# Kernel tuning notes

Measured on AMD Instinct MI355X. Metric: run time of the kernel, lower is better.

## Reference

```python
import jax, jax.numpy as jnp
import numpy as np

B, L, C = 32, 4096, 512
H = 8            # num_heads
WS = 16          # window size
HID = 4 * C      # mlp hidden
D = C // H       # head dim
SCALE = D ** -0.5
EPS = 1e-3       # keras LayerNormalization default epsilon


def _ln(x, g, b):
    m = jnp.mean(x, axis=-1, keepdims=True)
    v = jnp.var(x, axis=-1, keepdims=True)
    return (x - m) * jax.lax.rsqrt(v + EPS) * g + b


def setup_inputs() -> dict:
    key = jax.random.key(0)
    ks = jax.random.split(key, 12)
    s = 0.02
    return {
        "x": jax.random.normal(ks[0], (B, L, C), dtype=jnp.float32),
        "g1": jnp.ones((C,), jnp.float32),
        "b1": jnp.zeros((C,), jnp.float32),
        "w_qkv": jax.random.normal(ks[1], (C, 3 * C), jnp.float32) * s,
        "b_qkv": jnp.zeros((3 * C,), jnp.float32),
        "bias_table": jax.random.normal(ks[2], (2 * WS - 1, H), jnp.float32) * s,
        "w_proj": jax.random.normal(ks[3], (C, C), jnp.float32) * s,
        "b_proj": jnp.zeros((C,), jnp.float32),
        "g2": jnp.ones((C,), jnp.float32),
        "b2": jnp.zeros((C,), jnp.float32),
        "w_fc1": jax.random.normal(ks[4], (C, HID), jnp.float32) * s,
        "b_fc1": jnp.zeros((HID,), jnp.float32),
        "w_fc2": jax.random.normal(ks[5], (HID, C), jnp.float32) * s,
        "b_fc2": jnp.zeros((C,), jnp.float32),
    }


def reference(x, g1, b1, w_qkv, b_qkv, bias_table, w_proj, b_proj,
              g2, b2, w_fc1, b_fc1, w_fc2, b_fc2):
    shortcut = x
    h = _ln(x, g1, b1)
    # window partition: (B, L, C) -> (B*L/WS, WS, C); shift_size=0 so no roll
    xw = h.reshape(-1, WS, C)
    # qkv projection
    qkv = (xw @ w_qkv + b_qkv).reshape(-1, WS, 3, H, D)
    qkv = jnp.transpose(qkv, (2, 0, 3, 1, 4))  # (3, nB, H, WS, D)
    q, k, v = qkv[0] * SCALE, qkv[1], qkv[2]
    attn = jnp.einsum('bhqd,bhkd->bhqk', q, k)
    # relative position bias
    rel_idx = jnp.arange(WS)[:, None] - jnp.arange(WS)[None, :] + WS - 1  # (WS, WS)
    bias = jnp.transpose(bias_table[rel_idx], (2, 0, 1))  # (H, WS, WS)
    attn = jax.nn.softmax(attn + bias[None], axis=-1)
    out = jnp.einsum('bhqk,bhkd->bqhd', attn, v).reshape(-1, WS, C)
    out = out @ w_proj + b_proj
    # window reverse
    out = out.reshape(B, L, C)
    x = shortcut + out
    # MLP block (exact gelu matches tf.nn.gelu default approximate=False)
    h2 = _ln(x, g2, b2)
    h2 = jax.nn.gelu(h2 @ w_fc1 + b_fc1, approximate=False)
    h2 = h2 @ w_fc2 + b_fc2
    return x + h2
```

## Files before the change

kernel.cpp:

```cpp
#include <hip/hip_runtime.h>
#include <hip/hip_bf16.h>

typedef short bf16x8 __attribute__((ext_vector_type(8)));
typedef float f32x4 __attribute__((ext_vector_type(4)));

#define GLDS16(gp, lp)                                                         \
  __builtin_amdgcn_global_load_lds(                                            \
      (const __attribute__((address_space(1))) void*)(gp),                     \
      (__attribute__((address_space(3))) void*)(lp), 16, 0, 0)

static __device__ __forceinline__ unsigned short f2bf(float f) {
  unsigned u = __float_as_uint(f);
  u += 0x7fffu + ((u >> 16) & 1u);
  return (unsigned short)(u >> 16);
}

__global__ __launch_bounds__(256) void wt_transpose_kernel(
    const float* __restrict__ w, unsigned short* __restrict__ wt, int K, int N) {
  __shared__ float tile[32][33];
  const int n0 = blockIdx.x * 32, k0 = blockIdx.y * 32;
  const int tx = threadIdx.x & 31, ty = threadIdx.x >> 5;
#pragma unroll
  for (int i = 0; i < 4; ++i) {
    const int k = ty + i * 8;
    tile[k][tx] = w[(size_t)(k0 + k) * N + n0 + tx];
  }
  __syncthreads();
#pragma unroll
  for (int i = 0; i < 4; ++i) {
    const int n = ty + i * 8;
    wt[(size_t)(n0 + n) * K + k0 + tx] = f2bf(tile[tx][n]);
  }
}

__global__ __launch_bounds__(256) void ln_bf16_kernel(
    const float* __restrict__ x, const float* __restrict__ gw,
    const float* __restrict__ bw, unsigned short* __restrict__ out) {
  const int wv = threadIdx.x >> 6, lane = threadIdx.x & 63;
  const size_t t = (size_t)blockIdx.x * 4 + wv;
  const float4* xr = (const float4*)(x + t * 512);
  const float4 v0 = xr[lane * 2];
  const float4 v1 = xr[lane * 2 + 1];
  float s = v0.x + v0.y + v0.z + v0.w + v1.x + v1.y + v1.z + v1.w;
  float ss = v0.x * v0.x + v0.y * v0.y + v0.z * v0.z + v0.w * v0.w +
             v1.x * v1.x + v1.y * v1.y + v1.z * v1.z + v1.w * v1.w;
#pragma unroll
  for (int m = 1; m < 64; m <<= 1) {
    s += __shfl_xor(s, m);
    ss += __shfl_xor(ss, m);
  }
  const float mean = s * (1.0f / 512.0f);
  const float var = fmaxf(ss * (1.0f / 512.0f) - mean * mean, 0.0f);
  const float rstd = rsqrtf(var + 1e-3f);
  const float4* gp = (const float4*)gw;
  const float4* bp = (const float4*)bw;
  const float4 g0 = gp[lane * 2], g1 = gp[lane * 2 + 1];
  const float4 b0 = bp[lane * 2], b1 = bp[lane * 2 + 1];
  uint4 o;
  o.x = (unsigned)f2bf((v0.x - mean) * rstd * g0.x + b0.x) |
        ((unsigned)f2bf((v0.y - mean) * rstd * g0.y + b0.y) << 16);
  o.y = (unsigned)f2bf((v0.z - mean) * rstd * g0.z + b0.z) |
        ((unsigned)f2bf((v0.w - mean) * rstd * g0.w + b0.w) << 16);
  o.z = (unsigned)f2bf((v1.x - mean) * rstd * g1.x + b1.x) |
        ((unsigned)f2bf((v1.y - mean) * rstd * g1.y + b1.y) << 16);
  o.w = (unsigned)f2bf((v1.z - mean) * rstd * g1.z + b1.z) |
        ((unsigned)f2bf((v1.w - mean) * rstd * g1.w + b1.w) << 16);
  *(uint4*)(out + t * 512 + lane * 8) = o;
}

template <int EPI>
__global__ __launch_bounds__(256) void gemm_bf16_kernel(
    const unsigned short* __restrict__ A, const unsigned short* __restrict__ Bt,
    const float* __restrict__ bias, const float* __restrict__ resid,
    void* __restrict__ outv, int M, int N, int K) {
  __shared__ __align__(16) unsigned short sA[128 * 64];
  __shared__ __align__(16) unsigned short sB[128 * 64];
  const int nTn = N >> 7;
  const int nwg = gridDim.x;
  const int bid = blockIdx.x;
  const int swz = (bid & 7) * (nwg >> 3) + (bid >> 3);
  const int tm = swz / nTn, tn = swz % nTn;
  const int lane = threadIdx.x & 63, wv = threadIdx.x >> 6;
  const int wm = wv >> 1, wn = wv & 1;
  const int lr = lane & 15, lg = lane >> 4;
  const unsigned short* Ab =
      A + (size_t)tm * 128 * K + (size_t)(lane >> 3) * K + (lane & 7) * 8;
  const unsigned short* Bb =
      Bt + (size_t)tn * 128 * K + (size_t)(lane >> 3) * K + (lane & 7) * 8;
  f32x4 acc[4][4] = {};
  for (int kt = 0; kt < K; kt += 64) {
#pragma unroll
    for (int i = 0; i < 4; ++i) {
      const int r0 = (wv * 4 + i) * 8;
      GLDS16(Ab + (size_t)r0 * K + kt, &sA[r0 * 64]);
      GLDS16(Bb + (size_t)r0 * K + kt, &sB[r0 * 64]);
    }
    __syncthreads();
#pragma unroll
    for (int kk = 0; kk < 2; ++kk) {
      bf16x8 af[4], bf[4];
#pragma unroll
      for (int m = 0; m < 4; ++m)
        af[m] = *(const bf16x8*)&sA[(wm * 64 + m * 16 + lr) * 64 + kk * 32 + lg * 8];
#pragma unroll
      for (int n = 0; n < 4; ++n)
        bf[n] = *(const bf16x8*)&sB[(wn * 64 + n * 16 + lr) * 64 + kk * 32 + lg * 8];
#pragma unroll
      for (int m = 0; m < 4; ++m)
#pragma unroll
        for (int n = 0; n < 4; ++n)
          acc[m][n] = __builtin_amdgcn_mfma_f32_16x16x32_bf16(af[m], bf[n],
                                                              acc[m][n], 0, 0, 0);
    }
    __syncthreads();
  }
  const int row0 = tm * 128 + wm * 64 + lg * 4;
  const int col0 = tn * 128 + wn * 64 + lr;
#pragma unroll
  for (int n = 0; n < 4; ++n) {
    const int col = col0 + n * 16;
    const float bs = bias[col];
#pragma unroll
    for (int m = 0; m < 4; ++m) {
#pragma unroll
      for (int r = 0; r < 4; ++r) {
        const size_t idx = (size_t)(row0 + m * 16 + r) * N + col;
        float v = acc[m][n][r] + bs;
        if (EPI == 1) {
          ((float*)outv)[idx] = v + resid[idx];
        } else if (EPI == 2) {
          v = 0.5f * v * (1.0f + erff(v * 0.70710678118f));
          ((unsigned short*)outv)[idx] = f2bf(v);
        } else {
          ((unsigned short*)outv)[idx] = f2bf(v);
        }
      }
    }
  }
}

__global__ __launch_bounds__(256) void attn_kernel(
    const unsigned short* __restrict__ qkv,
    const float* __restrict__ bias_table, unsigned short* __restrict__ out) {
  __shared__ __align__(16) unsigned short sVt[4][64 * 16];
  __shared__ __align__(16) unsigned short sP[4][16 * 16];
  const int wv = threadIdx.x >> 6, lane = threadIdx.x & 63;
  const int task = blockIdx.x * 4 + wv;
  const int w = task >> 3, h = task & 7;
  const int c = lane & 15, g = lane >> 4;
  const unsigned short* base =
      qkv + (size_t)w * 16 * 1536 + (size_t)c * 1536 + h * 64;
  const bf16x8 qf0 = *(const bf16x8*)(base + g * 8);
  const bf16x8 qf1 = *(const bf16x8*)(base + 32 + g * 8);
  const bf16x8 kf0 = *(const bf16x8*)(base + 512 + g * 8);
  const bf16x8 kf1 = *(const bf16x8*)(base + 512 + 32 + g * 8);
  const bf16x8 vf0 = *(const bf16x8*)(base + 1024 + g * 8);
  const bf16x8 vf1 = *(const bf16x8*)(base + 1024 + 32 + g * 8);
  unsigned short* vt = sVt[wv];
#pragma unroll
  for (int j = 0; j < 8; ++j) vt[(g * 8 + j) * 16 + c] = (unsigned short)vf0[j];
#pragma unroll
  for (int j = 0; j < 8; ++j) vt[(32 + g * 8 + j) * 16 + c] = (unsigned short)vf1[j];
  f32x4 s = {0.f, 0.f, 0.f, 0.f};
  s = __builtin_amdgcn_mfma_f32_16x16x32_bf16(qf0, kf0, s, 0, 0, 0);
  s = __builtin_amdgcn_mfma_f32_16x16x32_bf16(qf1, kf1, s, 0, 0, 0);
  float p[4];
#pragma unroll
  for (int r = 0; r < 4; ++r) {
    const int q = g * 4 + r;
    p[r] = s[r] * 0.125f + bias_table[(q - c + 15) * 8 + h];
  }
#pragma unroll
  for (int r = 0; r < 4; ++r) {
    float m = p[r];
    m = fmaxf(m, __shfl_xor(m, 1));
    m = fmaxf(m, __shfl_xor(m, 2));
    m = fmaxf(m, __shfl_xor(m, 4));
    m = fmaxf(m, __shfl_xor(m, 8));
    const float e = __expf(p[r] - m);
    float t = e;
    t += __shfl_xor(t, 1);
    t += __shfl_xor(t, 2);
    t += __shfl_xor(t, 4);
    t += __shfl_xor(t, 8);
    p[r] = e * __builtin_amdgcn_rcpf(t);
  }
  unsigned short* pb = sP[wv];
#pragma unroll
  for (int r = 0; r < 4; ++r) pb[(g * 4 + r) * 16 + c] = f2bf(p[r]);
  __syncthreads();
  bf16x8 pf;
#pragma unroll
  for (int j = 0; j < 8; ++j) pf[j] = 0;
  if (g < 2) pf = *(const bf16x8*)&pb[c * 16 + g * 8];
  const int kk0 = (g & 1) * 8;
  unsigned short* ob = out + (size_t)w * 16 * 512 + (size_t)c * 512 + h * 64;
#pragma unroll
  for (int ch = 0; ch < 4; ++ch) {
    const bf16x8 av = *(const bf16x8*)&vt[(ch * 16 + c) * 16 + kk0];
    f32x4 o = {0.f, 0.f, 0.f, 0.f};
    o = __builtin_amdgcn_mfma_f32_16x16x32_bf16(av, pf, o, 0, 0, 0);
    ushort4 pk;
    pk.x = f2bf(o[0]);
    pk.y = f2bf(o[1]);
    pk.z = f2bf(o[2]);
    pk.w = f2bf(o[3]);
    *(ushort4*)(ob + ch * 16 + g * 4) = pk;
  }
}

extern "C" void kernel_launch(void* const* d_in, const int* in_sizes, int n_in,
                              void* d_out, int out_size, void* d_ws,
                              size_t ws_size, hipStream_t stream) {
  (void)in_sizes; (void)n_in; (void)out_size;
  const float* x      = (const float*)d_in[0];
  const float* g1     = (const float*)d_in[1];
  const float* b1     = (const float*)d_in[2];
  const float* w_qkv  = (const float*)d_in[3];
  const float* b_qkv  = (const float*)d_in[4];
  const float* btab   = (const float*)d_in[5];
  const float* w_proj = (const float*)d_in[6];
  const float* b_proj = (const float*)d_in[7];
  const float* g2     = (const float*)d_in[8];
  const float* b2     = (const float*)d_in[9];
  const float* w_fc1  = (const float*)d_in[10];
  const float* b_fc1  = (const float*)d_in[11];
  const float* w_fc2  = (const float*)d_in[12];
  const float* b_fc2  = (const float*)d_in[13];
  float* out = (float*)d_out;

  char* ws = (char*)d_ws;
  const size_t OFF_BIG = 134217728ull;
  const size_t OFF_ATT = OFF_BIG + 402653184ull;
  const size_t OFF_WT  = OFF_BIG + 536870912ull;
  if (ws_size < OFF_WT + 6291456ull) return;
  unsigned short* hbuf   = (unsigned short*)(ws);
  unsigned short* qkvhid = (unsigned short*)(ws + OFF_BIG);
  unsigned short* attnb  = (unsigned short*)(ws + OFF_ATT);
  unsigned short* wqkvT  = (unsigned short*)(ws + OFF_WT);
  unsigned short* wprojT = wqkvT + 512 * 1536;
  unsigned short* wfc1T  = wprojT + 512 * 512;
  unsigned short* wfc2T  = wfc1T + 512 * 2048;

  wt_transpose_kernel<<<dim3(1536 / 32, 512 / 32), 256, 0, stream>>>(w_qkv, wqkvT, 512, 1536);
  wt_transpose_kernel<<<dim3(512 / 32, 512 / 32), 256, 0, stream>>>(w_proj, wprojT, 512, 512);
  wt_transpose_kernel<<<dim3(2048 / 32, 512 / 32), 256, 0, stream>>>(w_fc1, wfc1T, 512, 2048);
  wt_transpose_kernel<<<dim3(512 / 32, 2048 / 32), 256, 0, stream>>>(w_fc2, wfc2T, 2048, 512);

  ln_bf16_kernel<<<32768, 256, 0, stream>>>(x, g1, b1, hbuf);
  gemm_bf16_kernel<0><<<12288, 256, 0, stream>>>(hbuf, wqkvT, b_qkv, nullptr,
                                                 qkvhid, 131072, 1536, 512);
  attn_kernel<<<16384, 256, 0, stream>>>(qkvhid, btab, attnb);
  gemm_bf16_kernel<1><<<4096, 256, 0, stream>>>(attnb, wprojT, b_proj, x, out,
                                                131072, 512, 512);
  ln_bf16_kernel<<<32768, 256, 0, stream>>>(out, g2, b2, hbuf);
  gemm_bf16_kernel<2><<<16384, 256, 0, stream>>>(hbuf, wfc1T, b_fc1, nullptr,
                                                 qkvhid, 131072, 2048, 512);
  gemm_bf16_kernel<1><<<4096, 256, 0, stream>>>(qkvhid, wfc2T, b_fc2, out, out,
                                                131072, 512, 2048);
}
```

Measured before the change: 2.363 ms.

## Replace 128x128 GEMM with 256x256 double-buffered, swizzled 8-wave pipelined kernel

```diff
diff --git a/kernel.cpp b/kernel.cpp
--- a/kernel.cpp
+++ b/kernel.cpp
@@ -8,6 +8,10 @@
   __builtin_amdgcn_global_load_lds(                                            \
       (const __attribute__((address_space(1))) void*)(gp),                     \
       (__attribute__((address_space(3))) void*)(lp), 16, 0, 0)
+#define BAR() __builtin_amdgcn_s_barrier()
+#define SCHED0() __builtin_amdgcn_sched_barrier(0)
+#define PRIO(p) __builtin_amdgcn_s_setprio(p)
+#define MFMA(a, b, c) __builtin_amdgcn_mfma_f32_16x16x32_bf16((a), (b), (c), 0, 0, 0)
 
 static __device__ __forceinline__ unsigned short f2bf(float f) {
   unsigned u = __float_as_uint(f);
@@ -69,59 +73,145 @@
 }
 
 template <int EPI>
-__global__ __launch_bounds__(256) void gemm_bf16_kernel(
+__global__ __launch_bounds__(512, 2) void gemm256_kernel(
     const unsigned short* __restrict__ A, const unsigned short* __restrict__ Bt,
     const float* __restrict__ bias, const float* __restrict__ resid,
     void* __restrict__ outv, int M, int N, int K) {
-  __shared__ __align__(16) unsigned short sA[128 * 64];
-  __shared__ __align__(16) unsigned short sB[128 * 64];
-  const int nTn = N >> 7;
-  const int nwg = gridDim.x;
-  const int bid = blockIdx.x;
+  __shared__ __align__(16) unsigned short lds[2][2][256 * 64];
+  const int NT = K >> 6;
+  const int nTn = N >> 8;
+  const int bid = blockIdx.x, nwg = gridDim.x;
   const int swz = (bid & 7) * (nwg >> 3) + (bid >> 3);
-  const int tm = swz / nTn, tn = swz % nTn;
-  const int lane = threadIdx.x & 63, wv = threadIdx.x >> 6;
-  const int wm = wv >> 1, wn = wv & 1;
-  const int lr = lane & 15, lg = lane >> 4;
-  const unsigned short* Ab =
-      A + (size_t)tm * 128 * K + (size_t)(lane >> 3) * K + (lane & 7) * 8;
-  const unsigned short* Bb =
-      Bt + (size_t)tn * 128 * K + (size_t)(lane >> 3) * K + (lane & 7) * 8;
-  f32x4 acc[4][4] = {};
-  for (int kt = 0; kt < K; kt += 64) {
-#pragma unroll
-    for (int i = 0; i < 4; ++i) {
-      const int r0 = (wv * 4 + i) * 8;
-      GLDS16(Ab + (size_t)r0 * K + kt, &sA[r0 * 64]);
-      GLDS16(Bb + (size_t)r0 * K + kt, &sB[r0 * 64]);
-    }
-    __syncthreads();
-#pragma unroll
-    for (int kk = 0; kk < 2; ++kk) {
-      bf16x8 af[4], bf[4];
-#pragma unroll
-      for (int m = 0; m < 4; ++m)
-        af[m] = *(const bf16x8*)&sA[(wm * 64 + m * 16 + lr) * 64 + kk * 32 + lg * 8];
-#pragma unroll
-      for (int n = 0; n < 4; ++n)
-        bf[n] = *(const bf16x8*)&sB[(wn * 64 + n * 16 + lr) * 64 + kk * 32 + lg * 8];
-#pragma unroll
-      for (int m = 0; m < 4; ++m)
-#pragma unroll
-        for (int n = 0; n < 4; ++n)
-          acc[m][n] = __builtin_amdgcn_mfma_f32_16x16x32_bf16(af[m], bf[n],
-                                                              acc[m][n], 0, 0, 0);
-    }
-    __syncthreads();
-  }
-  const int row0 = tm * 128 + wm * 64 + lg * 4;
-  const int col0 = tn * 128 + wn * 64 + lr;
+  const int tmr = (swz / nTn) * 256, tnr = (swz % nTn) * 256;
+  const int tid = threadIdx.x;
+  const int l = tid & 63, w = tid >> 6;
+  const int lr = l & 15, lg = l >> 4, x = lr & 7;
+  const int wm = w >> 2, wn = w & 3;
+  const int l8 = l >> 3;
+  const int coff = ((l & 7) ^ l8) * 8;
+  const int k0 = (lg ^ x) * 8, k1 = k0 ^ 32;
+  const int abase = (wm * 128 + lr) * 64;
+  const int bbase = (wn * 64 + lr) * 64;
+
+  f32x4 acc[8][4] = {};
+
+#define STAGE_A(buf, row0, kt)                                                  \
+  do {                                                                          \
+    const int kte_ = (kt) < NT ? (kt) : (kt) - NT;                              \
+    const unsigned short* s_ =                                                  \
+        A + (size_t)(tmr + (row0) + w * 16 + l8) * K + kte_ * 64 + coff;        \
+    GLDS16(s_, &lds[buf][0][((row0) + w * 16) * 64]);                           \
+    GLDS16(s_ + (size_t)8 * K, &lds[buf][0][((row0) + w * 16 + 8) * 64]);       \
+  } while (0)
+#define STAGE_B(buf, row0, kt)                                                  \
+  do {                                                                          \
+    const int kte_ = (kt) < NT ? (kt) : (kt) - NT;                              \
+    const unsigned short* s_ =                                                  \
+        Bt + (size_t)(tnr + (row0) + w * 16 + l8) * K + kte_ * 64 + coff;       \
+    GLDS16(s_, &lds[buf][1][((row0) + w * 16) * 64]);                           \
+    GLDS16(s_ + (size_t)8 * K, &lds[buf][1][((row0) + w * 16 + 8) * 64]);       \
+  } while (0)
+
+  STAGE_A(0, 0, 0);
+  STAGE_B(0, 0, 0);
+  STAGE_A(0, 128, 0);
+  STAGE_B(0, 128, 0);
+  STAGE_A(1, 0, 1);
+  STAGE_B(1, 0, 1);
+  asm volatile("s_waitcnt vmcnt(4)" ::: "memory");
+  BAR();
+  SCHED0();
+
+  for (int g = 0; g < NT; ++g) {
+    const int cb = g & 1, nb = cb ^ 1;
+    const unsigned short* sA = &lds[cb][0][0];
+    const unsigned short* sB = &lds[cb][1][0];
+    bf16x8 a0[4][2], a1[4][2], b0[2][2], b1[2][2];
+#pragma unroll
+    for (int m = 0; m < 4; ++m) {
+      a0[m][0] = *(const bf16x8*)(sA + abase + m * 1024 + k0);
+      a0[m][1] = *(const bf16x8*)(sA + abase + m * 1024 + k1);
+    }
+#pragma unroll
+    for (int n = 0; n < 2; ++n) {
+      b0[n][0] = *(const bf16x8*)(sB + bbase + n * 1024 + k0);
+      b0[n][1] = *(const bf16x8*)(sB + bbase + n * 1024 + k1);
+    }
+    STAGE_A(nb, 128, g + 1);
+    BAR();
+    PRIO(1);
+#pragma unroll
+    for (int m = 0; m < 4; ++m)
+#pragma unroll
+      for (int n = 0; n < 2; ++n) {
+        acc[m][n] = MFMA(a0[m][0], b0[n][0], acc[m][n]);
+        acc[m][n] = MFMA(a0[m][1], b0[n][1], acc[m][n]);
+      }
+    PRIO(0);
+    BAR();
+    SCHED0();
+#pragma unroll
+    for (int n = 0; n < 2; ++n) {
+      b1[n][0] = *(const bf16x8*)(sB + bbase + 2048 + n * 1024 + k0);
+      b1[n][1] = *(const bf16x8*)(sB + bbase + 2048 + n * 1024 + k1);
+    }
+    STAGE_B(nb, 128, g + 1);
+    BAR();
+    PRIO(1);
+#pragma unroll
+    for (int m = 0; m < 4; ++m)
+#pragma unroll
+      for (int n = 0; n < 2; ++n) {
+        acc[m][2 + n] = MFMA(a0[m][0], b1[n][0], acc[m][2 + n]);
+        acc[m][2 + n] = MFMA(a0[m][1], b1[n][1], acc[m][2 + n]);
+      }
+    PRIO(0);
+    BAR();
+    SCHED0();
+#pragma unroll
+    for (int m = 0; m < 4; ++m) {
+      a1[m][0] = *(const bf16x8*)(sA + abase + 4096 + m * 1024 + k0);
+      a1[m][1] = *(const bf16x8*)(sA + abase + 4096 + m * 1024 + k1);
+    }
+    BAR();
+    PRIO(1);
+#pragma unroll
+    for (int m = 0; m < 4; ++m)
+#pragma unroll
+      for (int n = 0; n < 2; ++n) {
+        acc[4 + m][2 + n] = MFMA(a1[m][0], b1[n][0], acc[4 + m][2 + n]);
+        acc[4 + m][2 + n] = MFMA(a1[m][1], b1[n][1], acc[4 + m][2 + n]);
+      }
+    PRIO(0);
+    BAR();
+    SCHED0();
+    STAGE_A(cb, 0, g + 2);
+    STAGE_B(cb, 0, g + 2);
+    asm volatile("s_waitcnt vmcnt(4)" ::: "memory");
+    BAR();
+    PRIO(1);
+#pragma unroll
+    for (int m = 0; m < 4; ++m)
+#pragma unroll
+      for (int n = 0; n < 2; ++n) {
+        acc[4 + m][n] = MFMA(a1[m][0], b0[n][0], acc[4 + m][n]);
+        acc[4 + m][n] = MFMA(a1[m][1], b0[n][1], acc[4 + m][n]);
+      }
+    PRIO(0);
+    BAR();
+    SCHED0();
+  }
+#undef STAGE_A
+#undef STAGE_B
+
+  const int row0 = tmr + wm * 128 + lg * 4;
+  const int col0 = tnr + wn * 64 + lr;
 #pragma unroll
   for (int n = 0; n < 4; ++n) {
     const int col = col0 + n * 16;
     const float bs = bias[col];
 #pragma unroll
-    for (int m = 0; m < 4; ++m) {
+    for (int m = 0; m < 8; ++m) {
 #pragma unroll
       for (int r = 0; r < 4; ++r) {
         const size_t idx = (size_t)(row0 + m * 16 + r) * N + col;
@@ -162,8 +252,8 @@
 #pragma unroll
   for (int j = 0; j < 8; ++j) vt[(32 + g * 8 + j) * 16 + c] = (unsigned short)vf1[j];
   f32x4 s = {0.f, 0.f, 0.f, 0.f};
-  s = __builtin_amdgcn_mfma_f32_16x16x32_bf16(qf0, kf0, s, 0, 0, 0);
-  s = __builtin_amdgcn_mfma_f32_16x16x32_bf16(qf1, kf1, s, 0, 0, 0);
+  s = MFMA(qf0, kf0, s);
+  s = MFMA(qf1, kf1, s);
   float p[4];
 #pragma unroll
   for (int r = 0; r < 4; ++r) {
@@ -199,7 +289,7 @@
   for (int ch = 0; ch < 4; ++ch) {
     const bf16x8 av = *(const bf16x8*)&vt[(ch * 16 + c) * 16 + kk0];
     f32x4 o = {0.f, 0.f, 0.f, 0.f};
-    o = __builtin_amdgcn_mfma_f32_16x16x32_bf16(av, pf, o, 0, 0, 0);
+    o = MFMA(av, pf, o);
     ushort4 pk;
     pk.x = f2bf(o[0]);
     pk.y = f2bf(o[1]);
@@ -248,14 +338,14 @@
   wt_transpose_kernel<<<dim3(512 / 32, 2048 / 32), 256, 0, stream>>>(w_fc2, wfc2T, 2048, 512);
 
   ln_bf16_kernel<<<32768, 256, 0, stream>>>(x, g1, b1, hbuf);
-  gemm_bf16_kernel<0><<<12288, 256, 0, stream>>>(hbuf, wqkvT, b_qkv, nullptr,
-                                                 qkvhid, 131072, 1536, 512);
+  gemm256_kernel<0><<<3072, 512, 0, stream>>>(hbuf, wqkvT, b_qkv, nullptr,
+                                              qkvhid, 131072, 1536, 512);
   attn_kernel<<<16384, 256, 0, stream>>>(qkvhid, btab, attnb);
-  gemm_bf16_kernel<1><<<4096, 256, 0, stream>>>(attnb, wprojT, b_proj, x, out,
-                                                131072, 512, 512);
+  gemm256_kernel<1><<<1024, 512, 0, stream>>>(attnb, wprojT, b_proj, x, out,
+                                              131072, 512, 512);
   ln_bf16_kernel<<<32768, 256, 0, stream>>>(out, g2, b2, hbuf);
-  gemm_bf16_kernel<2><<<16384, 256, 0, stream>>>(hbuf, wfc1T, b_fc1, nullptr,
-                                                 qkvhid, 131072, 2048, 512);
-  gemm_bf16_kernel<1><<<4096, 256, 0, stream>>>(qkvhid, wfc2T, b_fc2, out, out,
-                                                131072, 512, 2048);
-}
+  gemm256_kernel<2><<<4096, 512, 0, stream>>>(hbuf, wfc1T, b_fc1, nullptr,
+                                              qkvhid, 131072, 2048, 512);
+  gemm256_kernel<1><<<1024, 512, 0, stream>>>(qkvhid, wfc2T, b_fc2, out, out,
+                                              131072, 512, 2048);
+}
```

After: 1.981 ms. 1.19x faster.
